# Kernel optimization log

Measured on AMD Instinct MI355X. Metric: run time of the kernel, lower is better.

Reference implementation:

```python
import jax, jax.numpy as jnp
import numpy as np
from jax import lax

IN_CH, OC, NUM_LAYER = 6, 16, 256
ENC_DIM = OC * 4  # 64
DECODE_LEN = 23
FLAT = 5184


def _conv3d(x, w, b):
    # x: (B,C,D,H,W), w: (O,I,3,3,3), padding 1, stride 1
    y = lax.conv_general_dilated(x, w, window_strides=(1, 1, 1),
                                 padding=((1, 1), (1, 1), (1, 1)),
                                 dimension_numbers=('NCDHW', 'OIDHW', 'NCDHW'))
    return y + b[None, :, None, None, None]


def _maxpool(x):
    # MaxPool3d kernel (2,2,1) stride (2,2,1) over (D,H,W)
    return lax.reduce_window(x, -jnp.inf, lax.max,
                             (1, 1, 2, 2, 1), (1, 1, 2, 2, 1), 'VALID')


def setup_inputs() -> dict:
    key = jax.random.key(0)
    ks = jax.random.split(key, 24)
    n = lambda k, s: jax.random.normal(k, s, dtype=jnp.float32) * 0.05
    z = lambda s: jnp.zeros(s, dtype=jnp.float32)
    return {
        'x': jax.random.normal(ks[0], (512, IN_CH, 24, 72, 3), dtype=jnp.float32),
        'w1': n(ks[1], (OC, IN_CH, 3, 3, 3)), 'b1': z((OC,)),
        'w2': n(ks[2], (OC * 2, OC, 3, 3, 3)), 'b2': z((OC * 2,)),
        'w3': n(ks[3], (OC * 4, OC * 2, 3, 3, 3)), 'b3': z((OC * 4,)),
        'wih1': n(ks[4], (NUM_LAYER, ENC_DIM)), 'whh1': n(ks[5], (NUM_LAYER, NUM_LAYER)),
        'bih1': z((NUM_LAYER,)), 'bhh1': z((NUM_LAYER,)),
        'wih2': n(ks[6], (NUM_LAYER, NUM_LAYER)), 'whh2': n(ks[7], (NUM_LAYER, NUM_LAYER)),
        'bih2': z((NUM_LAYER,)), 'bhh2': z((NUM_LAYER,)),
        'w_init_h': n(ks[8], (NUM_LAYER, ENC_DIM)), 'b_init_h': z((NUM_LAYER,)),
        'w_init_h2': n(ks[9], (NUM_LAYER, NUM_LAYER)), 'b_init_h2': z((NUM_LAYER,)),
        'w_fc': n(ks[10], (1, NUM_LAYER)), 'b_fc': z((1,)),
        'w_lin1': n(ks[11], (NUM_LAYER, FLAT)), 'b_lin1': z((NUM_LAYER,)),
        'w_lin2': n(ks[12], (12, NUM_LAYER)), 'b_lin2': z((12,)),
    }


def reference(x, w1, b1, w2, b2, w3, b3,
              wih1, whh1, bih1, bhh1, wih2, whh2, bih2, bhh2,
              w_init_h, b_init_h, w_init_h2, b_init_h2,
              w_fc, b_fc, w_lin1, b_lin1, w_lin2, b_lin2):
    # Encoder: three conv+relu+pool stages (dropout is identity at p=0.0)
    out = _maxpool(jax.nn.relu(_conv3d(x, w1, b1)))
    out = _maxpool(jax.nn.relu(_conv3d(out, w2, b2)))
    out = _maxpool(jax.nn.relu(_conv3d(out, w3, b3)))  # (B, 64, 3, 9, 3)
    out = out.transpose(0, 2, 3, 4, 1)  # (B, D, H, W, C)
    B, C = out.shape[0], out.shape[-1]
    enc = out.reshape(B, -1, C)
    mean_enc = enc.mean(axis=1)  # (B, enc_dim)

    h = mean_enc @ w_init_h.T + b_init_h
    h2 = h @ w_init_h2.T + b_init_h2

    # Precompute the input-to-hidden projection once (constant across steps)
    ih_const = mean_enc @ wih1.T + bih1 + bhh1

    def step(carry, _):
        h, h2 = carry
        h_new = jnp.tanh(ih_const + h @ whh1.T)
        h2_new = jnp.tanh(h_new @ wih2.T + bih2 + h2 @ whh2.T + bhh2)
        pred = h2_new @ w_fc.T + b_fc  # (B, 1)
        return (h_new, h2_new), pred

    _, preds = lax.scan(step, (h, h2), None, length=DECODE_LEN)  # (T, B, 1)
    predictions = preds.transpose(1, 0, 2)  # (B, 23, 1)

    flat = out.reshape(B, -1)  # (B, 5184) in permuted (D,H,W,C) order, same as torch
    out_c = jnp.tanh(flat @ w_lin1.T + b_lin1) @ w_lin2.T + b_lin2  # (B, 12)
    return predictions, out_c
```

## Files before the change

### kernel.cpp

```cpp
#include <hip/hip_runtime.h>
#include <hip/hip_bf16.h>

typedef __attribute__((ext_vector_type(8))) short short8;
typedef __attribute__((ext_vector_type(4))) short short4_t;
typedef __attribute__((ext_vector_type(4))) float floatx4;

#define OFF_B1P   0
#define OFF_B2P   1792
#define OFF_B3P   8960
#define OFF_WIHT  36608
#define OFF_WIH1T 52992
#define OFF_WI2B  69376
#define OFF_WHH1B 134912
#define OFF_WIH2B 167680
#define OFF_WHH2B 200448
#define OFF_WL1P  233216
#define OFF_ME    896768
#define OFF_H0BF  929536
#define OFF_H2    1060608
#define OFF_IHC   1191680
#define OFF_P1    1322752
#define OFF_T1    1322752
#define OFF_Y     2377728
#define OFF_HSEQ  5392384
#define OFF_P2    6631168
#define OFF_P3BF  9285376

#define S2_H 88
#define S2_D 1760
#define S3_H 88
#define S3_D 1760
#define S3_HALF 14080

static __device__ inline short f2bf(float f) {
  union { __hip_bfloat16 h; short s; } u;
  u.h = __float2bfloat16(f);
  return u.s;
}
static __device__ inline float bf2f(short s) {
  union { unsigned u; float f; } v;
  v.u = ((unsigned)(unsigned short)s) << 16;
  return v.f;
}
static __device__ inline float fast_tanh(float x) {
  float e = __expf(2.f * x);
  return __builtin_fmaf(-2.f, __builtin_amdgcn_rcpf(e + 1.f), 1.f);
}

__global__ __launch_bounds__(256) void prep_kernel(
    const float* __restrict__ w1, const float* __restrict__ w2, const float* __restrict__ w3,
    const float* __restrict__ w_init_h, const float* __restrict__ wih1,
    const float* __restrict__ w_init_h2, const float* __restrict__ whh1,
    const float* __restrict__ wih2, const float* __restrict__ whh2,
    float* __restrict__ ws) {
  int i = blockIdx.x * 256 + threadIdx.x;
  if (i < 3584) {
    int j = i & 7, l = (i >> 3) & 63, c = i >> 9;
    int k = c*32 + ((l >> 4) << 3) + j;
    int tap = k >> 3, icp = k & 7, oc = l & 15;
    float v = (tap < 27 && icp < 6) ? w1[(oc*6 + icp)*27 + tap] : 0.f;
    ((__hip_bfloat16*)(ws + OFF_B1P))[i] = __float2bfloat16(v);
    return;
  }
  i -= 3584;
  if (i < 14336) {
    int j = i & 7, l = (i >> 3) & 63, cc = i >> 9;
    int c = cc % 14, nt = cc / 14;
    int k = c*32 + ((l >> 4) << 3) + j;
    int tap = k >> 4, ic = k & 15, oc = nt*16 + (l & 15);
    float v = (tap < 27) ? w2[(oc*16 + ic)*27 + tap] : 0.f;
    ((__hip_bfloat16*)(ws + OFF_B2P))[i] = __float2bfloat16(v);
    return;
  }
  i -= 14336;
  if (i < 55296) {
    int j = i & 7, l = (i >> 3) & 63, cc = i >> 9;
    int c = cc % 27, nt = cc / 27;
    int k = c*32 + ((l >> 4) << 3) + j;
    int ic = k & 31, oc = nt*16 + (l & 15);
    ((__hip_bfloat16*)(ws + OFF_B3P))[i] = __float2bfloat16(w3[(oc*32 + ic)*27 + c]);
    return;
  }
  i -= 55296;
  if (i < 16384) { int t = i & 255, k = i >> 8; ws[OFF_WIHT + i]  = w_init_h[t*64 + k];  return; }
  i -= 16384;
  if (i < 16384) { int t = i & 255, k = i >> 8; ws[OFF_WIH1T + i] = wih1[t*64 + k];      return; }
  i -= 16384;
  if (i < 65536) { ((__hip_bfloat16*)(ws + OFF_WI2B))[i] = __float2bfloat16(w_init_h2[i]); return; }
  i -= 65536;
  if (i < 65536) { ((__hip_bfloat16*)(ws + OFF_WHH1B))[i] = __float2bfloat16(whh1[i]); return; }
  i -= 65536;
  if (i < 65536) { ((__hip_bfloat16*)(ws + OFF_WIH2B))[i] = __float2bfloat16(wih2[i]); return; }
  i -= 65536;
  if (i < 65536) { ((__hip_bfloat16*)(ws + OFF_WHH2B))[i] = __float2bfloat16(whh2[i]); return; }
}

__global__ __launch_bounds__(256) void conv1_mfma(
    const float* __restrict__ x, const short* __restrict__ b1p,
    const float* __restrict__ bias, short* __restrict__ p1,
    const float* __restrict__ w_lin1, short* __restrict__ wl1p) {
  __shared__ __align__(16) short slab[8 * 74 * 5 * 8];
  int tid = threadIdx.x;
  if (blockIdx.x >= 2048) {
    int u = (blockIdx.x - 2048)*256 + tid;
    int l = u & 63, cc = u >> 6;
    int c = cc % 162, nt = cc / 162;
    int n = nt*16 + (l & 15);
    int k0 = c*32 + ((l >> 4) << 3);
    const float* src = w_lin1 + (size_t)n*5184 + k0;
    float4 v0 = *(const float4*)src;
    float4 v1 = *(const float4*)(src + 4);
    short8 s;
    s[0] = f2bf(v0.x); s[1] = f2bf(v0.y); s[2] = f2bf(v0.z); s[3] = f2bf(v0.w);
    s[4] = f2bf(v1.x); s[5] = f2bf(v1.y); s[6] = f2bf(v1.z); s[7] = f2bf(v1.w);
    *(short8*)(wl1p + (size_t)u*8) = s;
    return;
  }
  int b = blockIdx.x >> 2, q = blockIdx.x & 3;
  short8 z8 = {0,0,0,0,0,0,0,0};
  for (int i = tid; i < 2960; i += 256) *(short8*)(slab + i*8) = z8;
  __syncthreads();
  #pragma unroll
  for (int base = 0; base < 432; base += 256) {
    int u = base + tid;
    if (u < 432) {
      int dslot = u / 54;
      int g = u - dslot*54;
      int d = 6*q - 1 + dslot;
      if ((unsigned)d < 24u) {
        float4 v[6];
        #pragma unroll
        for (int ic = 0; ic < 6; ++ic)
          v[ic] = *(const float4*)(x + ((size_t)(b*6 + ic)*24 + d)*216 + g*4);
        const float* vv = (const float*)v;
        #pragma unroll
        for (int e = 0; e < 4; ++e) {
          int p = g*4 + e;
          int h = p/3, w = p - h*3;
          short8 s = z8;
          #pragma unroll
          for (int ic = 0; ic < 6; ++ic) s[ic] = f2bf(vv[ic*4 + e]);
          int slot = dslot*370 + (1 + h)*5 + (1 + w);
          slot ^= (slot >> 3) & 7;
          *(short8*)(slab + slot*8) = s;
        }
      }
    }
  }
  int lane = tid & 63, wid = tid >> 6;
  int quad = lane >> 4, col = lane & 15;
  short8 bf[7];
  #pragma unroll
  for (int c = 0; c < 7; ++c) bf[c] = *(const short8*)(b1p + (c*64 + lane)*8);
  int tapslot[7];
  #pragma unroll
  for (int c = 0; c < 7; ++c) {
    int tap = c*4 + quad;
    int tt = tap < 27 ? tap : 26;
    int kd = tt/9, rr = tt - kd*9, kh = rr/3, kw = rr - kh*3;
    tapslot[c] = (kd*74 + kh)*5 + kw;
  }
  float bv = bias[col];
  __syncthreads();
  for (int tile = wid; tile < 81; tile += 4) {
    int m = tile*16 + col;
    int dd = m & 1, dh = (m >> 1) & 1;
    int P = m >> 2;
    int t2 = P/3; int w = P - t2*3;
    int pdl = t2/36; int ph = t2 - pdl*36;
    int sbase = ((2*pdl + dd)*74 + 2*ph + dh)*5 + w;
    floatx4 acc = {0.f, 0.f, 0.f, 0.f};
    #pragma unroll
    for (int c = 0; c < 7; ++c) {
      int s = sbase + tapslot[c];
      s ^= (s >> 3) & 7;
      short8 af = *(const short8*)(slab + s*8);
      acc = __builtin_amdgcn_mfma_f32_16x16x32_bf16(af, bf[c], acc, 0, 0, 0);
    }
    float v = fmaxf(fmaxf(acc[0], acc[1]), fmaxf(acc[2], acc[3]));
    v = fmaxf(v + bv, 0.f);
    int Pout = q*324 + tile*4 + quad;
    p1[((size_t)b*1296 + Pout)*16 + col] = f2bf(v);
  }
}

__global__ __launch_bounds__(256) void conv2_mfma(
    const short* __restrict__ p1, const short* __restrict__ b2p,
    const float* __restrict__ bias2, short* __restrict__ p2g) {
  __shared__ __align__(16) short slab[14 * S2_D];
  int tid = threadIdx.x;
  int b = blockIdx.x >> 1, qh = blockIdx.x & 1;
  short8 z8 = {0,0,0,0,0,0,0,0};
  for (int i = tid; i < 3080; i += 256) *(short8*)(slab + i*8) = z8;
  __syncthreads();
  for (int i = tid; i < 1440; i += 256) {
    int c8 = i % 6; int r = i / 6; int hr = r % 20; int d = r / 20;
    int hg = 18*qh - 1 + hr;
    if ((unsigned)hg < 36u) {
      short8 v = *(const short8*)(p1 + ((size_t)b*1296 + (d*36 + hg)*3)*16 + c8*8);
      *(short8*)(slab + (d+1)*S2_D + hr*S2_H + 16 + c8*8) = v;
    }
  }
  int lane = tid & 63, wid = tid >> 6;
  int quad = lane >> 4, col = lane & 15;
  short8 bf[2][14];
  #pragma unroll
  for (int nt = 0; nt < 2; ++nt)
    #pragma unroll
    for (int c = 0; c < 14; ++c)
      bf[nt][c] = *(const short8*)(b2p + ((nt*14 + c)*64 + lane)*8);
  int tq = quad >> 1, icoff = (quad & 1) * 8;
  int tapoff[14];
  #pragma unroll
  for (int c = 0; c < 14; ++c) {
    int tap = 2*c + tq; if (tap > 26) tap = 26;
    int kd = tap/9, rr = tap - kd*9, kh = rr/3, kw = rr - kh*3;
    tapoff[c] = kd*S2_D + kh*S2_H + kw*16 + icoff;
  }
  float bv0 = bias2[col], bv1 = bias2[16 + col];
  __syncthreads();
  for (int tile = wid; tile < 41; tile += 4) {
    int m = tile*16 + col; if (m > 647) m = 647;
    int dd = m & 1, dh = (m >> 1) & 1;
    int P = m >> 2;
    int t = P/3; int w = P - t*3;
    int pd = t/9; int phl = t - pd*9;
    int base = (2*pd + dd)*S2_D + (2*phl + dh)*S2_H + w*16;
    floatx4 a0 = {0.f,0.f,0.f,0.f}, a1 = {0.f,0.f,0.f,0.f};
    #pragma unroll
    for (int c = 0; c < 14; ++c) {
      short8 a = *(const short8*)(slab + base + tapoff[c]);
      a0 = __builtin_amdgcn_mfma_f32_16x16x32_bf16(a, bf[0][c], a0, 0, 0, 0);
      a1 = __builtin_amdgcn_mfma_f32_16x16x32_bf16(a, bf[1][c], a1, 0, 0, 0);
    }
    int P2l = tile*4 + quad;
    if (P2l < 162) {
      float v0 = fmaxf(fmaxf(fmaxf(a0[0],a0[1]), fmaxf(a0[2],a0[3])) + bv0, 0.f);
      float v1 = fmaxf(fmaxf(fmaxf(a1[0],a1[1]), fmaxf(a1[2],a1[3])) + bv1, 0.f);
      int t2 = P2l/3; int w2 = P2l - t2*3;
      int pd2 = t2/9; int ph2 = t2 - pd2*9;
      size_t off = ((size_t)b*324 + (pd2*18 + 9*qh + ph2)*3 + w2)*32;
      p2g[off + col] = f2bf(v0);
      p2g[off + 16 + col] = f2bf(v1);
    }
  }
}

__global__ __launch_bounds__(256) void conv3_mfma(
    const short* __restrict__ p2g, const short* __restrict__ b3p,
    const float* __restrict__ bias3,
    short* __restrict__ p3bf, float* __restrict__ me) {
  __shared__ __align__(16) short slab[2 * S3_HALF];
  __shared__ float smean[4][32];
  int tid = threadIdx.x;
  int b = blockIdx.x;
  short8 z8 = {0,0,0,0,0,0,0,0};
  for (int i = tid; i < 3520; i += 256) *(short8*)(slab + i*8) = z8;
  __syncthreads();
  for (int i = tid; i < 1296; i += 256) {
    int c8 = i & 1;
    int hv = (i >> 1) & 1;
    int cell = i >> 2;
    int t = cell/3; int w = cell - t*3;
    int d = t/18; int h = t - d*18;
    short8 v = *(const short8*)(p2g + ((size_t)b*324 + cell)*32 + hv*16 + c8*8);
    *(short8*)(slab + hv*S3_HALF + (d+1)*S3_D + (h+1)*S3_H + (w+1)*16 + c8*8) = v;
  }
  int lane = tid & 63, wid = tid >> 6;
  int quad = lane >> 4, col = lane & 15;
  int ntp = (wid & 1) * 2;
  int tsel = wid >> 1;
  short8 bf[2][27];
  #pragma unroll
  for (int u = 0; u < 2; ++u)
    #pragma unroll
    for (int c = 0; c < 27; ++c)
      bf[u][c] = *(const short8*)(b3p + (((ntp+u)*27 + c)*64 + lane)*8);
  const short* sb = slab + (quad >> 1)*S3_HALF + (quad & 1)*8;
  float bva = bias3[ntp*16 + col], bvb = bias3[(ntp+1)*16 + col];
  float ms0 = 0.f, ms1 = 0.f;
  __syncthreads();
  for (int tile = tsel; tile < 21; tile += 2) {
    int m = tile*16 + col; if (m > 323) m = 323;
    int dd = m & 1, dh = (m >> 1) & 1;
    int P = m >> 2;
    int t = P/3; int w = P - t*3;
    int pd = t/9; int ph = t - pd*9;
    const short* ap = sb + (2*pd + dd)*S3_D + (2*ph + dh)*S3_H + w*16;
    floatx4 a0 = {0.f,0.f,0.f,0.f}, a1 = {0.f,0.f,0.f,0.f};
    #pragma unroll
    for (int c = 0; c < 27; ++c) {
      const int kd = c/9, rr = c - kd*9, kh = rr/3, kw = rr - kh*3;
      short8 a = *(const short8*)(ap + kd*S3_D + kh*S3_H + kw*16);
      a0 = __builtin_amdgcn_mfma_f32_16x16x32_bf16(a, bf[0][c], a0, 0, 0, 0);
      a1 = __builtin_amdgcn_mfma_f32_16x16x32_bf16(a, bf[1][c], a1, 0, 0, 0);
    }
    int Pout = tile*4 + quad;
    if (Pout < 81) {
      float v0 = fmaxf(fmaxf(fmaxf(a0[0],a0[1]), fmaxf(a0[2],a0[3])) + bva, 0.f);
      float v1 = fmaxf(fmaxf(fmaxf(a1[0],a1[1]), fmaxf(a1[2],a1[3])) + bvb, 0.f);
      size_t oi = ((size_t)b*81 + Pout)*64 + ntp*16 + col;
      p3bf[oi] = f2bf(v0);
      p3bf[oi + 16] = f2bf(v1);
      ms0 += v0; ms1 += v1;
    }
  }
  ms0 += __shfl_xor(ms0, 16, 64); ms0 += __shfl_xor(ms0, 32, 64);
  ms1 += __shfl_xor(ms1, 16, 64); ms1 += __shfl_xor(ms1, 32, 64);
  if (lane < 16) { smean[wid][lane] = ms0; smean[wid][16 + lane] = ms1; }
  __syncthreads();
  if (tid < 64) {
    float s = (tid < 32) ? (smean[0][tid] + smean[2][tid])
                         : (smean[1][tid-32] + smean[3][tid-32]);
    me[b*64 + tid] = s * (1.f / 81.f);
  }
}

__global__ __launch_bounds__(256) void init_kernel(
    const float* __restrict__ me, const float* __restrict__ wiht,
    const float* __restrict__ b_init_h, const float* __restrict__ wih1t,
    const float* __restrict__ bih1, const float* __restrict__ bhh1,
    short* __restrict__ h0bf, float* __restrict__ ihcout) {
  __shared__ float sme[2][64];
  int t = threadIdx.x; int bb = blockIdx.x * 2;
  if (t < 128) sme[t >> 6][t & 63] = me[(bb + (t >> 6))*64 + (t & 63)];
  __syncthreads();
  float a0 = b_init_h[t], a1 = a0;
  float c0 = bih1[t] + bhh1[t], c1 = c0;
  #pragma unroll
  for (int k = 0; k < 64; ++k) {
    float w1v = wiht[k*256 + t], w2v = wih1t[k*256 + t];
    a0 += sme[0][k]*w1v; a1 += sme[1][k]*w1v;
    c0 += sme[0][k]*w2v; c1 += sme[1][k]*w2v;
  }
  h0bf[(size_t)bb*256 + t]     = f2bf(a0);
  h0bf[(size_t)(bb+1)*256 + t] = f2bf(a1);
  ihcout[(size_t)bb*256 + t]     = c0;
  ihcout[(size_t)(bb+1)*256 + t] = c1;
}

__global__ __launch_bounds__(512) void fusedA(
    const short* __restrict__ h0bf, const float* __restrict__ ihc,
    const short* __restrict__ whh1b, short* __restrict__ hseq,
    const short* __restrict__ p3bf, const short* __restrict__ wl1p,
    const float* __restrict__ b_lin1, float* __restrict__ t1,
    const short* __restrict__ wi2b, const float* __restrict__ b_init_h2,
    float* __restrict__ h2out) {
  __shared__ __align__(16) short pool[23040];
  int tid = threadIdx.x;

  if (blockIdx.x >= 160) {
    short (*As)[72] = (short (*)[72])pool;
    short (*Bs)[72] = (short (*)[72])(pool + 4608);
    int lane = tid & 63, w = tid >> 6;
    int quad = lane >> 4, col = lane & 15;
    int m0 = (blockIdx.x - 160) * 64;
    int n0 = w * 32;
    float bv[2];
    #pragma unroll
    for (int t = 0; t < 2; ++t) bv[t] = b_init_h2[n0 + t*16 + col];
    floatx4 acc[4][2];
    #pragma unroll
    for (int ms = 0; ms < 4; ++ms)
      #pragma unroll
      for (int t = 0; t < 2; ++t)
        #pragma unroll
        for (int r = 0; r < 4; ++r) acc[ms][t][r] = bv[t];
    int arow = tid >> 3, achk = tid & 7;
    #pragma unroll 1
    for (int kr = 0; kr < 256; kr += 64) {
      short8 ra = *(const short8*)(h0bf + (size_t)(m0 + arow)*256 + kr + achk*8);
      short8 rb[4];
      #pragma unroll
      for (int p = 0; p < 4; ++p) {
        int idx = p*512 + tid;
        rb[p] = *(const short8*)(wi2b + (size_t)(idx >> 3)*256 + kr + (idx & 7)*8);
      }
      if (kr) __syncthreads();
      *(short8*)&As[arow][achk*8] = ra;
      #pragma unroll
      for (int p = 0; p < 4; ++p) {
        int idx = p*512 + tid;
        *(short8*)&Bs[idx >> 3][(idx & 7)*8] = rb[p];
      }
      __syncthreads();
      #pragma unroll
      for (int cc = 0; cc < 2; ++cc) {
        short8 bfr[2];
        #pragma unroll
        for (int t = 0; t < 2; ++t)
          bfr[t] = *(const short8*)&Bs[n0 + t*16 + col][cc*32 + quad*8];
        #pragma unroll
        for (int ms = 0; ms < 4; ++ms) {
          short8 afr = *(const short8*)&As[ms*16 + col][cc*32 + quad*8];
          acc[ms][0] = __builtin_amdgcn_mfma_f32_16x16x32_bf16(afr, bfr[0], acc[ms][0], 0, 0, 0);
          acc[ms][1] = __builtin_amdgcn_mfma_f32_16x16x32_bf16(afr, bfr[1], acc[ms][1], 0, 0, 0);
        }
      }
    }
    #pragma unroll
    for (int ms = 0; ms < 4; ++ms)
      #pragma unroll
      for (int t = 0; t < 2; ++t)
        #pragma unroll
        for (int r = 0; r < 4; ++r)
          h2out[(size_t)(m0 + ms*16 + quad*4 + r)*256 + n0 + t*16 + col] = acc[ms][t][r];
    return;
  }

  if (blockIdx.x >= 32) {
    short (*Ab)[512][8] = (short (*)[512][8])pool;
    short (*Bb)[512][8] = (short (*)[512][8])(pool + 8192);
    int sub = tid >> 8, stid = tid & 255;
    int lane = stid & 63, w = stid >> 6;
    int quad = lane >> 4, col = lane & 15;
    int idx = (blockIdx.x - 32)*2 + sub;
    int mt = idx & 7, ntb = (idx >> 3) & 3, kz = idx >> 5;
    int c0 = (kz <= 2) ? kz*22 : 44 + (kz - 2)*20;
    int cn = (kz < 2) ? 22 : ((kz == 7) ? 18 : 20);
    int Nr = cn >> 1;
    int m0 = mt*64;
    floatx4 acc[4];
    #pragma unroll
    for (int t = 0; t < 4; ++t) {
      float bv = (kz == 0) ? b_lin1[ntb*64 + t*16 + col] : 0.f;
      #pragma unroll
      for (int r = 0; r < 4; ++r) acc[t][r] = bv;
    }
    const short* asrc = p3bf + (size_t)(m0 + w*16 + col)*5184 + c0*32 + quad*8;
    const short* bsrc = wl1p + ((size_t)((ntb*4 + w)*162 + c0)*64 + lane)*8;
    short8 ra0 = *(const short8*)asrc;
    short8 ra1 = *(const short8*)(asrc + 32);
    short8 rb0 = *(const short8*)bsrc;
    short8 rb1 = *(const short8*)(bsrc + 512);
    asrc += 64; bsrc += 1024;
    #pragma unroll 1
    for (int r = 0; r < Nr; ++r) {
      *(short8*)&Ab[0][tid][0] = ra0;
      *(short8*)&Ab[1][tid][0] = ra1;
      *(short8*)&Bb[0][tid][0] = rb0;
      *(short8*)&Bb[1][tid][0] = rb1;
      if (r + 1 < Nr) {
        ra0 = *(const short8*)asrc;
        ra1 = *(const short8*)(asrc + 32);
        rb0 = *(const short8*)bsrc;
        rb1 = *(const short8*)(bsrc + 512);
        asrc += 64; bsrc += 1024;
      }
      __syncthreads();
      #pragma unroll
      for (int cc = 0; cc < 2; ++cc) {
        short8 a = *(const short8*)&Ab[cc][sub*256 + w*64 + lane][0];
        #pragma unroll
        for (int t = 0; t < 4; ++t) {
          short8 b = *(const short8*)&Bb[cc][sub*256 + t*64 + lane][0];
          acc[t] = __builtin_amdgcn_mfma_f32_16x16x32_bf16(a, b, acc[t], 0, 0, 0);
        }
      }
      __syncthreads();
    }
    float* to = t1 + (size_t)kz * 131072;
    #pragma unroll
    for (int t = 0; t < 4; ++t)
      #pragma unroll
      for (int r = 0; r < 4; ++r)
        to[(size_t)(m0 + w*16 + quad*4 + r)*256 + ntb*64 + t*16 + col] = acc[t][r];
    return;
  }

  short (*hbuf)[16][264] = (short (*)[16][264])pool;
  int lane = tid & 63, wid = tid >> 6;
  int quad = lane >> 4, col = lane & 15;
  int bb = blockIdx.x * 16;
  int n0 = wid * 32;
  short8 w1f[2][8];
  #pragma unroll
  for (int t = 0; t < 2; ++t)
    #pragma unroll
    for (int c = 0; c < 8; ++c)
      w1f[t][c] = *(const short8*)(whh1b + (n0 + t*16 + col)*256 + c*32 + quad*8);
  floatx4 ihcr[2];
  #pragma unroll
  for (int t = 0; t < 2; ++t) {
    float4 iv = *(const float4*)(ihc + (size_t)(bb + col)*256 + n0 + t*16 + quad*4);
    ihcr[t][0] = iv.x; ihcr[t][1] = iv.y; ihcr[t][2] = iv.z; ihcr[t][3] = iv.w;
  }
  #pragma unroll
  for (int t = 0; t < 2; ++t)
    #pragma unroll
    for (int c = 0; c < 8; ++c) asm volatile("" : "+v"(w1f[t][c]));

  {
    int m = tid >> 5, c = tid & 31;
    *(short8*)&hbuf[0][m][c*8] = *(const short8*)(h0bf + (size_t)(bb + m)*256 + c*8);
  }
  __syncthreads();
  #pragma unroll 1
  for (int i = 0; i < 23; ++i) {
    int cur = i & 1;
    floatx4 a1[2];
    #pragma unroll
    for (int t = 0; t < 2; ++t) {
      a1[t][0] = ihcr[t][0]; a1[t][1] = ihcr[t][1];
      a1[t][2] = ihcr[t][2]; a1[t][3] = ihcr[t][3];
    }
    #pragma unroll
    for (int c = 0; c < 8; ++c) {
      short8 hb = *(const short8*)&hbuf[cur][col][c*32 + quad*8];
      a1[0] = __builtin_amdgcn_mfma_f32_16x16x32_bf16(w1f[0][c], hb, a1[0], 0, 0, 0);
      a1[1] = __builtin_amdgcn_mfma_f32_16x16x32_bf16(w1f[1][c], hb, a1[1], 0, 0, 0);
    }
    #pragma unroll
    for (int t = 0; t < 2; ++t) {
      short4_t pk;
      #pragma unroll
      for (int r = 0; r < 4; ++r) pk[r] = f2bf(fast_tanh(a1[t][r]));
      *(short4_t*)&hbuf[cur ^ 1][col][n0 + t*16 + quad*4] = pk;
      *(short4_t*)(hseq + ((size_t)i*512 + bb + col)*256 + n0 + t*16 + quad*4) = pk;
    }
    __syncthreads();
  }
}

__global__ __launch_bounds__(512) void fusedB(
    const short* __restrict__ hseq, const short* __restrict__ wih2b,
    const float* __restrict__ bih2, const float* __restrict__ bhh2,
    float* __restrict__ yseq,
    const float* __restrict__ t1, const float* __restrict__ w_lin2,
    const float* __restrict__ b_lin2, float* __restrict__ outc) {
  __shared__ __align__(16) short As[64][72];
  __shared__ __align__(16) short Bs[256][72];
  __shared__ float st[16][257];
  int tid = threadIdx.x;

  if (blockIdx.x < 32) {
    int bb = blockIdx.x * 16;
    for (int i = tid; i < 4096; i += 512) {
      int m = i >> 8, k = i & 255;
      size_t i0 = (size_t)(bb + m)*256 + k;
      float s = 0.f;
      #pragma unroll
      for (int z = 0; z < 8; ++z) s += t1[i0 + (size_t)z*131072];
      st[m][k] = fast_tanh(s);
    }
    __syncthreads();
    if (tid < 192) {
      int r = tid / 12, j = tid % 12;
      float s = b_lin2[j];
      #pragma unroll 1
      for (int k = 0; k < 256; ++k) s += st[r][k] * w_lin2[j*256 + k];
      outc[(size_t)(bb + r)*12 + j] = s;
    }
    return;
  }

  int lane = tid & 63, w = tid >> 6;
  int quad = lane >> 4, col = lane & 15;
  int m0 = (blockIdx.x - 32) * 64;
  int n0 = w * 32;
  float bv[2];
  #pragma unroll
  for (int t = 0; t < 2; ++t) {
    int n = n0 + t*16 + col;
    bv[t] = bih2[n] + bhh2[n];
  }
  floatx4 acc[4][2];
  #pragma unroll
  for (int ms = 0; ms < 4; ++ms)
    #pragma unroll
    for (int t = 0; t < 2; ++t)
      #pragma unroll
      for (int r = 0; r < 4; ++r) acc[ms][t][r] = bv[t];
  int arow = tid >> 3, achk = tid & 7;
  #pragma unroll 1
  for (int kr = 0; kr < 256; kr += 64) {
    short8 ra = *(const short8*)(hseq + (size_t)(m0 + arow)*256 + kr + achk*8);
    short8 rb[4];
    #pragma unroll
    for (int p = 0; p < 4; ++p) {
      int idx = p*512 + tid;
      rb[p] = *(const short8*)(wih2b + (size_t)(idx >> 3)*256 + kr + (idx & 7)*8);
    }
    if (kr) __syncthreads();
    *(short8*)&As[arow][achk*8] = ra;
    #pragma unroll
    for (int p = 0; p < 4; ++p) {
      int idx = p*512 + tid;
      *(short8*)&Bs[idx >> 3][(idx & 7)*8] = rb[p];
    }
    __syncthreads();
    #pragma unroll
    for (int cc = 0; cc < 2; ++cc) {
      short8 bfr[2];
      #pragma unroll
      for (int t = 0; t < 2; ++t)
        bfr[t] = *(const short8*)&Bs[n0 + t*16 + col][cc*32 + quad*8];
      #pragma unroll
      for (int ms = 0; ms < 4; ++ms) {
        short8 afr = *(const short8*)&As[ms*16 + col][cc*32 + quad*8];
        acc[ms][0] = __builtin_amdgcn_mfma_f32_16x16x32_bf16(afr, bfr[0], acc[ms][0], 0, 0, 0);
        acc[ms][1] = __builtin_amdgcn_mfma_f32_16x16x32_bf16(afr, bfr[1], acc[ms][1], 0, 0, 0);
      }
    }
  }
  #pragma unroll
  for (int ms = 0; ms < 4; ++ms)
    #pragma unroll
    for (int t = 0; t < 2; ++t)
      #pragma unroll
      for (int r = 0; r < 4; ++r)
        yseq[(size_t)(m0 + ms*16 + quad*4 + r)*256 + n0 + t*16 + col] = acc[ms][t][r];
}

__global__ __launch_bounds__(512) void t_h2(
    const float* __restrict__ h2in, const float* __restrict__ yseq,
    const short* __restrict__ whh2b,
    const float* __restrict__ w_fc, const float* __restrict__ b_fc,
    float* __restrict__ preds) {
  __shared__ __align__(16) short h2buf[2][16][264];
  __shared__ float predsAll[23][8][16];
  int tid = threadIdx.x;
  int lane = tid & 63, wid = tid >> 6;
  int quad = lane >> 4, col = lane & 15;
  int bb = blockIdx.x * 16;
  int n0 = wid * 32;
  short8 w3f[2][8];
  #pragma unroll
  for (int t = 0; t < 2; ++t)
    #pragma unroll
    for (int c = 0; c < 8; ++c)
      w3f[t][c] = *(const short8*)(whh2b + (n0 + t*16 + col)*256 + c*32 + quad*8);
  float4 wfcv[2];
  #pragma unroll
  for (int t = 0; t < 2; ++t)
    wfcv[t] = *(const float4*)(w_fc + n0 + t*16 + quad*4);
  float bfc = b_fc[0];
  #pragma unroll
  for (int t = 0; t < 2; ++t)
    #pragma unroll
    for (int c = 0; c < 8; ++c) asm volatile("" : "+v"(w3f[t][c]));

  for (int i = tid; i < 4096; i += 512) {
    int m = i >> 8, k = i & 255;
    h2buf[0][m][k] = f2bf(h2in[(size_t)(bb + m)*256 + k]);
  }
  __syncthreads();
  #pragma unroll 1
  for (int i = 0; i < 23; ++i) {
    int cur = i & 1;
    float4 yv[2];
    #pragma unroll
    for (int t = 0; t < 2; ++t)
      yv[t] = *(const float4*)(yseq + ((size_t)i*512 + bb + col)*256 + n0 + t*16 + quad*4);
    floatx4 z0 = {0.f,0.f,0.f,0.f}, z1 = {0.f,0.f,0.f,0.f};
    #pragma unroll
    for (int c = 0; c < 8; ++c) {
      short8 gb = *(const short8*)&h2buf[cur][col][c*32 + quad*8];
      z0 = __builtin_amdgcn_mfma_f32_16x16x32_bf16(w3f[0][c], gb, z0, 0, 0, 0);
      z1 = __builtin_amdgcn_mfma_f32_16x16x32_bf16(w3f[1][c], gb, z1, 0, 0, 0);
    }
    float pr = 0.f;
    short4_t o0, o1;
    const float* y0p = (const float*)&yv[0];
    const float* y1p = (const float*)&yv[1];
    const float* wf0 = (const float*)&wfcv[0];
    const float* wf1 = (const float*)&wfcv[1];
    #pragma unroll
    for (int r = 0; r < 4; ++r) {
      float t0 = fast_tanh(z0[r] + y0p[r]);
      float t1 = fast_tanh(z1[r] + y1p[r]);
      o0[r] = f2bf(t0); o1[r] = f2bf(t1);
      pr += t0*wf0[r] + t1*wf1[r];
    }
    *(short4_t*)&h2buf[cur ^ 1][col][n0 + quad*4] = o0;
    *(short4_t*)&h2buf[cur ^ 1][col][n0 + 16 + quad*4] = o1;
    pr += __shfl_xor(pr, 16, 64);
    pr += __shfl_xor(pr, 32, 64);
    if (lane < 16) predsAll[i][wid][lane] = pr;
    __syncthreads();
  }
  if (tid < 16) {
    #pragma unroll 1
    for (int p = 0; p < 23; ++p) {
      float sv = bfc;
      #pragma unroll
      for (int w = 0; w < 8; ++w) sv += predsAll[p][w][tid];
      preds[(size_t)(bb + tid)*23 + p] = sv;
    }
  }
}

extern "C" void kernel_launch(void* const* d_in, const int* in_sizes, int n_in,
                              void* d_out, int out_size, void* d_ws, size_t ws_size,
                              hipStream_t stream) {
  const float* x         = (const float*)d_in[0];
  const float* w1        = (const float*)d_in[1];
  const float* b1        = (const float*)d_in[2];
  const float* w2        = (const float*)d_in[3];
  const float* b2        = (const float*)d_in[4];
  const float* w3        = (const float*)d_in[5];
  const float* b3        = (const float*)d_in[6];
  const float* wih1      = (const float*)d_in[7];
  const float* whh1      = (const float*)d_in[8];
  const float* bih1      = (const float*)d_in[9];
  const float* bhh1      = (const float*)d_in[10];
  const float* wih2      = (const float*)d_in[11];
  const float* whh2      = (const float*)d_in[12];
  const float* bih2      = (const float*)d_in[13];
  const float* bhh2      = (const float*)d_in[14];
  const float* w_init_h  = (const float*)d_in[15];
  const float* b_init_h  = (const float*)d_in[16];
  const float* w_init_h2 = (const float*)d_in[17];
  const float* b_init_h2 = (const float*)d_in[18];
  const float* w_fc      = (const float*)d_in[19];
  const float* b_fc      = (const float*)d_in[20];
  const float* w_lin1    = (const float*)d_in[21];
  const float* b_lin1    = (const float*)d_in[22];
  const float* w_lin2    = (const float*)d_in[23];
  const float* b_lin2    = (const float*)d_in[24];
  float* ws  = (float*)d_ws;
  float* out = (float*)d_out;

  prep_kernel<<<1438, 256, 0, stream>>>(w1, w2, w3, w_init_h, wih1, w_init_h2,
                                        whh1, wih2, whh2, ws);
  conv1_mfma<<<2696, 256, 0, stream>>>(x, (const short*)(ws + OFF_B1P), b1,
                                       (short*)(ws + OFF_P1),
                                       w_lin1, (short*)(ws + OFF_WL1P));
  conv2_mfma<<<1024, 256, 0, stream>>>((const short*)(ws + OFF_P1),
                                       (const short*)(ws + OFF_B2P), b2,
                                       (short*)(ws + OFF_P2));
  conv3_mfma<<<512, 256, 0, stream>>>((const short*)(ws + OFF_P2),
                                      (const short*)(ws + OFF_B3P), b3,
                                      (short*)(ws + OFF_P3BF), ws + OFF_ME);
  init_kernel<<<256, 256, 0, stream>>>(ws + OFF_ME, ws + OFF_WIHT, b_init_h,
                                       ws + OFF_WIH1T, bih1, bhh1,
                                       (short*)(ws + OFF_H0BF), ws + OFF_IHC);
  fusedA<<<168, 512, 0, stream>>>((const short*)(ws + OFF_H0BF), ws + OFF_IHC,
                                  (const short*)(ws + OFF_WHH1B),
                                  (short*)(ws + OFF_HSEQ),
                                  (const short*)(ws + OFF_P3BF),
                                  (const short*)(ws + OFF_WL1P),
                                  b_lin1, ws + OFF_T1,
                                  (const short*)(ws + OFF_WI2B), b_init_h2,
                                  ws + OFF_H2);
  fusedB<<<216, 512, 0, stream>>>((const short*)(ws + OFF_HSEQ),
                                  (const short*)(ws + OFF_WIH2B),
                                  bih2, bhh2, ws + OFF_Y,
                                  ws + OFF_T1, w_lin2, b_lin2, out + 11776);
  t_h2<<<32, 512, 0, stream>>>(ws + OFF_H2, ws + OFF_Y,
                               (const short*)(ws + OFF_WHH2B),
                               w_fc, b_fc, out);
}
```

Before: 292.5 us.

## Split conv1 blocks into two H-halves with smaller LDS slabs

Each conv1 block now covers half the H range (38 rows including halo) instead of the full 74, which doubles the block count and roughly halves shared memory per block, with remapped output indexing. The input XOR swizzle on LDS slots is removed in favor of plain indexing. The goal is higher occupancy and better load balance across CUs. The cost is redundant halo loads, more blocks, and possible LDS bank conflicts now that the swizzle is gone.

```diff
diff --git a/kernel.cpp b/kernel.cpp
--- a/kernel.cpp
+++ b/kernel.cpp
@@ -99,10 +99,10 @@
     const float* __restrict__ x, const short* __restrict__ b1p,
     const float* __restrict__ bias, short* __restrict__ p1,
     const float* __restrict__ w_lin1, short* __restrict__ wl1p) {
-  __shared__ __align__(16) short slab[8 * 74 * 5 * 8];
+  __shared__ __align__(16) short slab[8 * 38 * 5 * 8];
   int tid = threadIdx.x;
-  if (blockIdx.x >= 2048) {
-    int u = (blockIdx.x - 2048)*256 + tid;
+  if (blockIdx.x >= 4096) {
+    int u = (blockIdx.x - 4096)*256 + tid;
     int l = u & 63, cc = u >> 6;
     int c = cc % 162, nt = cc / 162;
     int n = nt*16 + (l & 15);
@@ -116,16 +116,15 @@
     *(short8*)(wl1p + (size_t)u*8) = s;
     return;
   }
-  int b = blockIdx.x >> 2, q = blockIdx.x & 3;
+  int bq = blockIdx.x >> 1, hh = blockIdx.x & 1;
+  int b = bq >> 2, q = bq & 3;
   short8 z8 = {0,0,0,0,0,0,0,0};
-  for (int i = tid; i < 2960; i += 256) *(short8*)(slab + i*8) = z8;
-  __syncthreads();
-  #pragma unroll
-  for (int base = 0; base < 432; base += 256) {
-    int u = base + tid;
-    if (u < 432) {
-      int dslot = u / 54;
-      int g = u - dslot*54;
+  for (int i = tid; i < 1520; i += 256) *(short8*)(slab + i*8) = z8;
+  __syncthreads();
+  {
+    int dslot = tid >> 5, gi = tid & 31;
+    if (gi < 28) {
+      int g = gi + (hh ? 26 : 0);
       int d = 6*q - 1 + dslot;
       if ((unsigned)d < 24u) {
         float4 v[6];
@@ -133,16 +132,18 @@
         for (int ic = 0; ic < 6; ++ic)
           v[ic] = *(const float4*)(x + ((size_t)(b*6 + ic)*24 + d)*216 + g*4);
         const float* vv = (const float*)v;
+        int hbase = 36*hh - 1;
         #pragma unroll
         for (int e = 0; e < 4; ++e) {
           int p = g*4 + e;
           int h = p/3, w = p - h*3;
-          short8 s = z8;
-          #pragma unroll
-          for (int ic = 0; ic < 6; ++ic) s[ic] = f2bf(vv[ic*4 + e]);
-          int slot = dslot*370 + (1 + h)*5 + (1 + w);
-          slot ^= (slot >> 3) & 7;
-          *(short8*)(slab + slot*8) = s;
+          int r = h - hbase;
+          if ((unsigned)r < 38u) {
+            short8 s = z8;
+            #pragma unroll
+            for (int ic = 0; ic < 6; ++ic) s[ic] = f2bf(vv[ic*4 + e]);
+            *(short8*)(slab + (dslot*190 + r*5 + 1 + w)*8) = s;
+          }
         }
       }
     }
@@ -158,29 +159,32 @@
     int tap = c*4 + quad;
     int tt = tap < 27 ? tap : 26;
     int kd = tt/9, rr = tt - kd*9, kh = rr/3, kw = rr - kh*3;
-    tapslot[c] = (kd*74 + kh)*5 + kw;
+    tapslot[c] = kd*190 + kh*5 + kw;
   }
   float bv = bias[col];
   __syncthreads();
-  for (int tile = wid; tile < 81; tile += 4) {
-    int m = tile*16 + col;
+  for (int tile = wid; tile < 41; tile += 4) {
+    int m = tile*16 + col; if (m > 647) m = 647;
     int dd = m & 1, dh = (m >> 1) & 1;
     int P = m >> 2;
     int t2 = P/3; int w = P - t2*3;
-    int pdl = t2/36; int ph = t2 - pdl*36;
-    int sbase = ((2*pdl + dd)*74 + 2*ph + dh)*5 + w;
+    int pdl = t2/18; int ph = t2 - pdl*18;
+    int sbase = (2*pdl + dd)*190 + (2*ph + dh)*5 + w;
     floatx4 acc = {0.f, 0.f, 0.f, 0.f};
     #pragma unroll
     for (int c = 0; c < 7; ++c) {
-      int s = sbase + tapslot[c];
-      s ^= (s >> 3) & 7;
-      short8 af = *(const short8*)(slab + s*8);
+      short8 af = *(const short8*)(slab + (sbase + tapslot[c])*8);
       acc = __builtin_amdgcn_mfma_f32_16x16x32_bf16(af, bf[c], acc, 0, 0, 0);
     }
     float v = fmaxf(fmaxf(acc[0], acc[1]), fmaxf(acc[2], acc[3]));
     v = fmaxf(v + bv, 0.f);
-    int Pout = q*324 + tile*4 + quad;
-    p1[((size_t)b*1296 + Pout)*16 + col] = f2bf(v);
+    int Pl = tile*4 + quad;
+    if (Pl < 162) {
+      int t2o = Pl/3; int wo = Pl - t2o*3;
+      int pdo = t2o/18; int pho = t2o - pdo*18;
+      int Pout = q*324 + hh*54 + pdo*108 + pho*3 + wo;
+      p1[((size_t)b*1296 + Pout)*16 + col] = f2bf(v);
+    }
   }
 }
 
@@ -723,7 +727,7 @@
 
   prep_kernel<<<1438, 256, 0, stream>>>(w1, w2, w3, w_init_h, wih1, w_init_h2,
                                         whh1, wih2, whh2, ws);
-  conv1_mfma<<<2696, 256, 0, stream>>>(x, (const short*)(ws + OFF_B1P), b1,
+  conv1_mfma<<<4744, 256, 0, stream>>>(x, (const short*)(ws + OFF_B1P), b1,
                                        (short*)(ws + OFF_P1),
                                        w_lin1, (short*)(ws + OFF_WL1P));
   conv2_mfma<<<1024, 256, 0, stream>>>((const short*)(ws + OFF_P1),
```

Result: faster. 282.8 us (-3.3%).
